# Performance work log

Measured on AMD Instinct MI355X. Metric: run time of the kernel, lower is better.

## Reference

```python
import jax, jax.numpy as jnp
import numpy as np

N_NODES = 50000


def _sage_layer(x, edges, W_neigh, W_self, b):
    """HeteroGraphConv(sum) of per-relation DGL SAGEConv(mean).

    x:        [N, F_in] node features (single node type)
    edges:    [R, 2, E] int (src, dst) per relation
    W_neigh:  [R, F_in, F_out], W_self: [R, F_in, F_out], b: [R, F_out]
    returns:  [N, F_out]
    """
    N = x.shape[0]
    R = edges.shape[0]
    out = jnp.zeros((N, W_neigh.shape[-1]), dtype=x.dtype)
    for r in range(R):  # small fixed number of relation types
        src = edges[r, 0]
        dst = edges[r, 1]
        # mean-aggregate neighbor features onto dst
        s = jax.ops.segment_sum(x[src], dst, num_segments=N)          # [N, F_in]
        deg = jax.ops.segment_sum(jnp.ones_like(dst, dtype=x.dtype), dst,
                                  num_segments=N)                     # [N]
        mean = s / jnp.maximum(deg, 1.0)[:, None]                     # zero-deg -> 0
        # SAGEConv(mean): fc_self(h_dst) + fc_neigh(mean_neigh) + bias
        out = out + x @ W_self[r] + mean @ W_neigh[r] + b[r]
    return out


def setup_inputs() -> dict:
    key = jax.random.key(0)
    ks = jax.random.split(key, 10)
    F_in, H, O, R, E = 128, 128, 64, 2, 800000
    scale_in = 1.0 / np.sqrt(F_in)
    scale_h = 1.0 / np.sqrt(H)
    return {
        "x": jax.random.normal(ks[0], (N_NODES, F_in), dtype=jnp.float32),
        "edges": jax.random.randint(ks[1], (R, 2, E), 0, N_NODES, dtype=jnp.int32),
        "neg_edges": jax.random.randint(ks[2], (2, E), 0, N_NODES, dtype=jnp.int32),
        "W_neigh1": jax.random.normal(ks[3], (R, F_in, H), jnp.float32) * scale_in,
        "W_self1": jax.random.normal(ks[4], (R, F_in, H), jnp.float32) * scale_in,
        "b1": jnp.zeros((R, H), jnp.float32),
        "W_neigh2": jax.random.normal(ks[5], (R, H, O), jnp.float32) * scale_h,
        "W_self2": jax.random.normal(ks[6], (R, H, O), jnp.float32) * scale_h,
        "b2": jnp.zeros((R, O), jnp.float32),
    }


def reference(x, edges, neg_edges, W_neigh1, W_self1, b1, W_neigh2, W_self2, b2):
    h = _sage_layer(x, edges, W_neigh1, W_self1, b1)
    h = jax.nn.relu(h)
    h = _sage_layer(h, edges, W_neigh2, W_self2, b2)          # [N, O]
    # HeteroDotProductPredictor: u_dot_v on edges of the scored etype (rel 0)
    pos_score = jnp.sum(h[edges[0, 0]] * h[edges[0, 1]], axis=-1)      # [E]
    neg_score = jnp.sum(h[neg_edges[0]] * h[neg_edges[1]], axis=-1)    # [E_neg]
    return pos_score, neg_score
```

## Files before the change

### kernel.cpp

```cpp
#include <hip/hip_runtime.h>


#define BW 128
#define NBK_MAX 1024
#define EPB 8192

typedef __attribute__((ext_vector_type(8))) short bf16x8;
typedef __attribute__((ext_vector_type(4))) float floatx4;

__device__ __forceinline__ unsigned short f2bf(float f) {
    unsigned u = __float_as_uint(f);
    unsigned r = u + 0x7FFFu + ((u >> 16) & 1u);
    return (unsigned short)(r >> 16);
}
__device__ __forceinline__ unsigned pack2(float a, float b) {
    return (unsigned)f2bf(a) | ((unsigned)f2bf(b) << 16);
}
__device__ __forceinline__ float bflo(unsigned v) { return __uint_as_float(v << 16); }
__device__ __forceinline__ float bfhi(unsigned v) { return __uint_as_float(v & 0xFFFF0000u); }
#define RFL(x) __builtin_amdgcn_readfirstlane(x)

__global__ __launch_bounds__(256) void
bucket_count_kernel(const int* __restrict__ edges, int* __restrict__ bcnt,
                    int NBK, int E)
{
    __shared__ int cnt[2 * NBK_MAX];
    const int rbT = 2 * NBK;
    const int t = threadIdx.x;
    for (int k = t; k < rbT; k += 256) cnt[k] = 0;
    __syncthreads();
    long long start = (long long)blockIdx.x * EPB;
    long long twoE = 2LL * E;
    for (int u = 0; u < EPB / 256; ++u) {
        long long idx = start + u * 256 + t;
        if (idx < twoE) {
            int r = idx >= E;
            int e = (int)(idx - (long long)r * E);
            int d = edges[(size_t)r * 2 * E + E + e];
            atomicAdd(&cnt[r * NBK + (d >> 7)], 1);
        }
    }
    __syncthreads();
    for (int k = t; k < rbT; k += 256)
        if (cnt[k]) atomicAdd(&bcnt[k], cnt[k]);
}

__global__ __launch_bounds__(1024) void
bucket_scan_kernel(const int* __restrict__ bcnt, int* __restrict__ bko,
                   int rbT, int twoE)
{
    __shared__ int sm[1024];
    int t = threadIdx.x;
    int v = (t < rbT) ? bcnt[t] : 0;
    sm[t] = v;
    __syncthreads();
    for (int s = 1; s < 1024; s <<= 1) {
        int u = (t >= s) ? sm[t - s] : 0;
        __syncthreads();
        sm[t] += u;
        __syncthreads();
    }
    if (t < rbT) bko[t] = sm[t] - v;
    if (t == 0) bko[rbT] = twoE;
}

__global__ __launch_bounds__(256) void
partition_kernel(const int* __restrict__ edges, const int* __restrict__ bko,
                 int* __restrict__ gcur, uint2* __restrict__ staging,
                 int NBK, int E)
{
    __shared__ int cnt[2 * NBK_MAX];
    __shared__ int base[2 * NBK_MAX];
    const int rbT = 2 * NBK;
    const int t = threadIdx.x;
    for (int k = t; k < rbT; k += 256) cnt[k] = 0;
    __syncthreads();
    long long start = (long long)blockIdx.x * EPB;
    long long twoE = 2LL * E;
    for (int u = 0; u < EPB / 256; ++u) {
        long long idx = start + u * 256 + t;
        if (idx < twoE) {
            int r = idx >= E;
            int e = (int)(idx - (long long)r * E);
            int d = edges[(size_t)r * 2 * E + E + e];
            atomicAdd(&cnt[r * NBK + (d >> 7)], 1);
        }
    }
    __syncthreads();
    for (int k = t; k < rbT; k += 256) {
        int c0 = cnt[k];
        if (c0) base[k] = bko[k] + atomicAdd(&gcur[k], c0);
        cnt[k] = 0;
    }
    __syncthreads();
    for (int u = 0; u < EPB / 256; ++u) {
        long long idx = start + u * 256 + t;
        if (idx < twoE) {
            int r = idx >= E;
            int e = (int)(idx - (long long)r * E);
            int s = edges[(size_t)r * 2 * E + e];
            int d = edges[(size_t)r * 2 * E + E + e];
            int rb = r * NBK + (d >> 7);
            int pos = atomicAdd(&cnt[rb], 1);
            staging[(size_t)base[rb] + pos] = make_uint2((unsigned)s, (unsigned)d);
        }
    }
}

__global__ __launch_bounds__(256) void
bucket_csr_kernel(const uint2* __restrict__ staging, const int* __restrict__ bko,
                  int* __restrict__ csr, int* __restrict__ off,
                  int NBK, int N)
{
    __shared__ int hist[BW], excl[BW], cur[BW], sc[BW];
    const int rb = blockIdx.x;
    const int r = rb / NBK;
    const int b = rb % NBK;
    const int node0 = b * BW;
    const int nn = min(BW, N - node0);
    const int cbase = bko[rb];
    const int c = bko[rb + 1] - cbase;
    const int t = threadIdx.x;

    if (t < BW) { hist[t] = 0; cur[t] = 0; }
    __syncthreads();
    for (int k = t; k < c; k += 256)
        atomicAdd(&hist[(int)staging[(size_t)cbase + k].y - node0], 1);
    __syncthreads();
    if (t < BW) sc[t] = hist[t];
    __syncthreads();
    for (int s = 1; s < BW; s <<= 1) {
        int v = (t < BW && t >= s) ? sc[t - s] : 0;
        __syncthreads();
        if (t < BW) sc[t] += v;
        __syncthreads();
    }
    if (t < BW) excl[t] = sc[t] - hist[t];
    if (t < nn) off[(size_t)r * N + node0 + t] = cbase + excl[t];
    __syncthreads();
    for (int k = t; k < c; k += 256) {
        uint2 pr = staging[(size_t)cbase + k];
        int l = (int)pr.y - node0;
        int pos = atomicAdd(&cur[l], 1);
        csr[(size_t)cbase + excl[l] + pos] = (int)pr.x;
    }
}

__global__ void cvt_kernel(const float* __restrict__ in,
                           unsigned short* __restrict__ o, int n4)
{
    int t = blockIdx.x * blockDim.x + threadIdx.x;
    if (t >= n4) return;
    float4 v = ((const float4*)in)[t];
    ushort4 r;
    r.x = f2bf(v.x); r.y = f2bf(v.y); r.z = f2bf(v.z); r.w = f2bf(v.w);
    ((ushort4*)o)[t] = r;
}

__global__ void prep_kernel(const float* __restrict__ Ws1, const float* __restrict__ Wn1,
                            const float* __restrict__ b1,
                            const float* __restrict__ Ws2, const float* __restrict__ Wn2,
                            const float* __restrict__ b2,
                            unsigned short* __restrict__ WT1z, unsigned short* __restrict__ WT1a,
                            unsigned short* __restrict__ WT1b, float* __restrict__ bc1,
                            unsigned short* __restrict__ WT2z, unsigned short* __restrict__ WT2a,
                            unsigned short* __restrict__ WT2b, float* __restrict__ bc2)
{
    int t = blockIdx.x * blockDim.x + threadIdx.x;
    if (t < 16384) {
        int n = t >> 7, k = t & 127;
        int in = k * 128 + n;
        WT1z[t] = f2bf(Ws1[in] + Ws1[16384 + in]);
        WT1a[t] = f2bf(Wn1[in]);
        WT1b[t] = f2bf(Wn1[16384 + in]);
    }
    if (t < 8192) {
        int n = t >> 7, k = t & 127;
        int in = k * 64 + n;
        WT2z[t] = f2bf(Ws2[in] + Ws2[8192 + in]);
        WT2a[t] = f2bf(Wn2[in]);
        WT2b[t] = f2bf(Wn2[8192 + in]);
    }
    if (t < 128) bc1[t] = b1[t] + b1[128 + t];
    if (t < 64)  bc2[t] = b2[t] + b2[64 + t];
}

__global__ __launch_bounds__(256) void
agg1_kernel(const unsigned short* __restrict__ xb,
            const int* __restrict__ csr, const int* __restrict__ off,
            unsigned short* __restrict__ m0, unsigned short* __restrict__ m1,
            int N, int twoE)
{
    int w = blockIdx.x * 4 + (threadIdx.x >> 6);
    int lane = threadIdx.x & 63;
    if (w >= N) return;
    const int col = lane * 2;
    const unsigned short* xc = xb + col;

    float sx0 = 0.f, sy0 = 0.f, sx1 = 0.f, sy1 = 0.f;

    int o0 = RFL(off[w]);
    int o1 = RFL(off[w + 1]);
    int d0 = o1 - o0;
    int j = o0;
    for (; j + 15 < o1; j += 16) {
        int s0 = RFL(csr[j]);      int s1 = RFL(csr[j + 1]);
        int s2 = RFL(csr[j + 2]);  int s3 = RFL(csr[j + 3]);
        int s4 = RFL(csr[j + 4]);  int s5 = RFL(csr[j + 5]);
        int s6 = RFL(csr[j + 6]);  int s7 = RFL(csr[j + 7]);
        int s8 = RFL(csr[j + 8]);  int s9 = RFL(csr[j + 9]);
        int sa = RFL(csr[j + 10]); int sb = RFL(csr[j + 11]);
        int sc = RFL(csr[j + 12]); int sd = RFL(csr[j + 13]);
        int se = RFL(csr[j + 14]); int sf = RFL(csr[j + 15]);
        unsigned a0 = *(const unsigned*)(xc + (size_t)s0 * 128);
        unsigned a1 = *(const unsigned*)(xc + (size_t)s1 * 128);
        unsigned a2 = *(const unsigned*)(xc + (size_t)s2 * 128);
        unsigned a3 = *(const unsigned*)(xc + (size_t)s3 * 128);
        unsigned a4 = *(const unsigned*)(xc + (size_t)s4 * 128);
        unsigned a5 = *(const unsigned*)(xc + (size_t)s5 * 128);
        unsigned a6 = *(const unsigned*)(xc + (size_t)s6 * 128);
        unsigned a7 = *(const unsigned*)(xc + (size_t)s7 * 128);
        unsigned a8 = *(const unsigned*)(xc + (size_t)s8 * 128);
        unsigned a9 = *(const unsigned*)(xc + (size_t)s9 * 128);
        unsigned aa = *(const unsigned*)(xc + (size_t)sa * 128);
        unsigned ab = *(const unsigned*)(xc + (size_t)sb * 128);
        unsigned ac = *(const unsigned*)(xc + (size_t)sc * 128);
        unsigned ad = *(const unsigned*)(xc + (size_t)sd * 128);
        unsigned ae = *(const unsigned*)(xc + (size_t)se * 128);
        unsigned af = *(const unsigned*)(xc + (size_t)sf * 128);
        sx0 += (((bflo(a0) + bflo(a1)) + (bflo(a2) + bflo(a3))) +
                ((bflo(a4) + bflo(a5)) + (bflo(a6) + bflo(a7)))) +
               (((bflo(a8) + bflo(a9)) + (bflo(aa) + bflo(ab))) +
                ((bflo(ac) + bflo(ad)) + (bflo(ae) + bflo(af))));
        sy0 += (((bfhi(a0) + bfhi(a1)) + (bfhi(a2) + bfhi(a3))) +
                ((bfhi(a4) + bfhi(a5)) + (bfhi(a6) + bfhi(a7)))) +
               (((bfhi(a8) + bfhi(a9)) + (bfhi(aa) + bfhi(ab))) +
                ((bfhi(ac) + bfhi(ad)) + (bfhi(ae) + bfhi(af))));
    }
    for (; j + 7 < o1; j += 8) {
        int s0 = RFL(csr[j]);     int s1 = RFL(csr[j + 1]);
        int s2 = RFL(csr[j + 2]); int s3 = RFL(csr[j + 3]);
        int s4 = RFL(csr[j + 4]); int s5 = RFL(csr[j + 5]);
        int s6 = RFL(csr[j + 6]); int s7 = RFL(csr[j + 7]);
        unsigned a0 = *(const unsigned*)(xc + (size_t)s0 * 128);
        unsigned a1 = *(const unsigned*)(xc + (size_t)s1 * 128);
        unsigned a2 = *(const unsigned*)(xc + (size_t)s2 * 128);
        unsigned a3 = *(const unsigned*)(xc + (size_t)s3 * 128);
        unsigned a4 = *(const unsigned*)(xc + (size_t)s4 * 128);
        unsigned a5 = *(const unsigned*)(xc + (size_t)s5 * 128);
        unsigned a6 = *(const unsigned*)(xc + (size_t)s6 * 128);
        unsigned a7 = *(const unsigned*)(xc + (size_t)s7 * 128);
        sx0 += ((bflo(a0) + bflo(a1)) + (bflo(a2) + bflo(a3))) +
               ((bflo(a4) + bflo(a5)) + (bflo(a6) + bflo(a7)));
        sy0 += ((bfhi(a0) + bfhi(a1)) + (bfhi(a2) + bfhi(a3))) +
               ((bfhi(a4) + bfhi(a5)) + (bfhi(a6) + bfhi(a7)));
    }
    for (; j < o1; ++j) {
        int s0 = RFL(csr[j]);
        unsigned a = *(const unsigned*)(xc + (size_t)s0 * 128);
        sx0 += bflo(a); sy0 += bfhi(a);
    }

    int p = N + w;
    o0 = RFL(off[p]);
    o1 = (p + 1 < 2 * N) ? RFL(off[p + 1]) : twoE;
    int d1 = o1 - o0;
    j = o0;
    for (; j + 15 < o1; j += 16) {
        int s0 = RFL(csr[j]);      int s1 = RFL(csr[j + 1]);
        int s2 = RFL(csr[j + 2]);  int s3 = RFL(csr[j + 3]);
        int s4 = RFL(csr[j + 4]);  int s5 = RFL(csr[j + 5]);
        int s6 = RFL(csr[j + 6]);  int s7 = RFL(csr[j + 7]);
        int s8 = RFL(csr[j + 8]);  int s9 = RFL(csr[j + 9]);
        int sa = RFL(csr[j + 10]); int sb = RFL(csr[j + 11]);
        int sc = RFL(csr[j + 12]); int sd = RFL(csr[j + 13]);
        int se = RFL(csr[j + 14]); int sf = RFL(csr[j + 15]);
        unsigned a0 = *(const unsigned*)(xc + (size_t)s0 * 128);
        unsigned a1 = *(const unsigned*)(xc + (size_t)s1 * 128);
        unsigned a2 = *(const unsigned*)(xc + (size_t)s2 * 128);
        unsigned a3 = *(const unsigned*)(xc + (size_t)s3 * 128);
        unsigned a4 = *(const unsigned*)(xc + (size_t)s4 * 128);
        unsigned a5 = *(const unsigned*)(xc + (size_t)s5 * 128);
        unsigned a6 = *(const unsigned*)(xc + (size_t)s6 * 128);
        unsigned a7 = *(const unsigned*)(xc + (size_t)s7 * 128);
        unsigned a8 = *(const unsigned*)(xc + (size_t)s8 * 128);
        unsigned a9 = *(const unsigned*)(xc + (size_t)s9 * 128);
        unsigned aa = *(const unsigned*)(xc + (size_t)sa * 128);
        unsigned ab = *(const unsigned*)(xc + (size_t)sb * 128);
        unsigned ac = *(const unsigned*)(xc + (size_t)sc * 128);
        unsigned ad = *(const unsigned*)(xc + (size_t)sd * 128);
        unsigned ae = *(const unsigned*)(xc + (size_t)se * 128);
        unsigned af = *(const unsigned*)(xc + (size_t)sf * 128);
        sx1 += (((bflo(a0) + bflo(a1)) + (bflo(a2) + bflo(a3))) +
                ((bflo(a4) + bflo(a5)) + (bflo(a6) + bflo(a7)))) +
               (((bflo(a8) + bflo(a9)) + (bflo(aa) + bflo(ab))) +
                ((bflo(ac) + bflo(ad)) + (bflo(ae) + bflo(af))));
        sy1 += (((bfhi(a0) + bfhi(a1)) + (bfhi(a2) + bfhi(a3))) +
                ((bfhi(a4) + bfhi(a5)) + (bfhi(a6) + bfhi(a7)))) +
               (((bfhi(a8) + bfhi(a9)) + (bfhi(aa) + bfhi(ab))) +
                ((bfhi(ac) + bfhi(ad)) + (bfhi(ae) + bfhi(af))));
    }
    for (; j + 7 < o1; j += 8) {
        int s0 = RFL(csr[j]);     int s1 = RFL(csr[j + 1]);
        int s2 = RFL(csr[j + 2]); int s3 = RFL(csr[j + 3]);
        int s4 = RFL(csr[j + 4]); int s5 = RFL(csr[j + 5]);
        int s6 = RFL(csr[j + 6]); int s7 = RFL(csr[j + 7]);
        unsigned a0 = *(const unsigned*)(xc + (size_t)s0 * 128);
        unsigned a1 = *(const unsigned*)(xc + (size_t)s1 * 128);
        unsigned a2 = *(const unsigned*)(xc + (size_t)s2 * 128);
        unsigned a3 = *(const unsigned*)(xc + (size_t)s3 * 128);
        unsigned a4 = *(const unsigned*)(xc + (size_t)s4 * 128);
        unsigned a5 = *(const unsigned*)(xc + (size_t)s5 * 128);
        unsigned a6 = *(const unsigned*)(xc + (size_t)s6 * 128);
        unsigned a7 = *(const unsigned*)(xc + (size_t)s7 * 128);
        sx1 += ((bflo(a0) + bflo(a1)) + (bflo(a2) + bflo(a3))) +
               ((bflo(a4) + bflo(a5)) + (bflo(a6) + bflo(a7)));
        sy1 += ((bfhi(a0) + bfhi(a1)) + (bfhi(a2) + bfhi(a3))) +
               ((bfhi(a4) + bfhi(a5)) + (bfhi(a6) + bfhi(a7)));
    }
    for (; j < o1; ++j) {
        int s0 = RFL(csr[j]);
        unsigned a = *(const unsigned*)(xc + (size_t)s0 * 128);
        sx1 += bflo(a); sy1 += bfhi(a);
    }

    float inv0 = 1.0f / fmaxf((float)d0, 1.0f);
    float inv1 = 1.0f / fmaxf((float)d1, 1.0f);
    *(unsigned*)(m0 + (size_t)w * 128 + col) = pack2(sx0 * inv0, sy0 * inv0);
    *(unsigned*)(m1 + (size_t)w * 128 + col) = pack2(sx1 * inv1, sy1 * inv1);
}

__global__ __launch_bounds__(256) void
gemm1_fused_kernel(const unsigned short* __restrict__ xb,
                   const unsigned short* __restrict__ m0,
                   const unsigned short* __restrict__ m1,
                   const unsigned short* __restrict__ WTz,
                   const unsigned short* __restrict__ WTa,
                   const unsigned short* __restrict__ WTb,
                   const float* __restrict__ bias,
                   unsigned short* __restrict__ h1b, int N)
{
    __shared__ float eb[64][129];

    const int tid = threadIdx.x;
    const int wave = tid >> 6;
    const int lane = tid & 63;
    const int m = lane & 15;
    const int quad = lane >> 4;

    floatx4 acc[8];
    const floatx4 z4 = {0.f, 0.f, 0.f, 0.f};
#pragma unroll
    for (int t = 0; t < 8; ++t) acc[t] = z4;

    int arow = blockIdx.x * 64 + wave * 16 + m;
    if (arow >= N) arow = N - 1;
    const size_t abase = (size_t)arow * 128 + quad * 8;

#pragma unroll
    for (int s = 0; s < 4; ++s) {
        bf16x8 ax = *(const bf16x8*)(xb + abase + s * 32);
        bf16x8 a0 = *(const bf16x8*)(m0 + abase + s * 32);
        bf16x8 a1 = *(const bf16x8*)(m1 + abase + s * 32);
#pragma unroll
        for (int t = 0; t < 8; ++t) {
            const size_t bo = (size_t)(t * 16 + m) * 128 + s * 32 + quad * 8;
            acc[t] = __builtin_amdgcn_mfma_f32_16x16x32_bf16(
                ax, *(const bf16x8*)(WTz + bo), acc[t], 0, 0, 0);
            acc[t] = __builtin_amdgcn_mfma_f32_16x16x32_bf16(
                a0, *(const bf16x8*)(WTa + bo), acc[t], 0, 0, 0);
            acc[t] = __builtin_amdgcn_mfma_f32_16x16x32_bf16(
                a1, *(const bf16x8*)(WTb + bo), acc[t], 0, 0, 0);
        }
    }

#pragma unroll
    for (int t = 0; t < 8; ++t)
#pragma unroll
        for (int i = 0; i < 4; ++i)
            eb[wave * 16 + quad * 4 + i][t * 16 + m] = acc[t][i];
    __syncthreads();

#pragma unroll
    for (int j = 0; j < 4; ++j) {
        int lr = wave * 16 + j * 4 + quad;
        int grow = blockIdx.x * 64 + lr;
        if (grow < N) {
#pragma unroll
            for (int i = 0; i < 2; ++i) {
                int c0 = (i * 16 + m) * 4;
                float v0 = fmaxf(eb[lr][c0 + 0] + bias[c0 + 0], 0.0f);
                float v1 = fmaxf(eb[lr][c0 + 1] + bias[c0 + 1], 0.0f);
                float v2 = fmaxf(eb[lr][c0 + 2] + bias[c0 + 2], 0.0f);
                float v3 = fmaxf(eb[lr][c0 + 3] + bias[c0 + 3], 0.0f);
                ushort4 u;
                u.x = f2bf(v0); u.y = f2bf(v1); u.z = f2bf(v2); u.w = f2bf(v3);
                *(ushort4*)(h1b + (size_t)grow * 128 + c0) = u;
            }
        }
    }
}

__global__ __launch_bounds__(256) void
gemm2_fused_kernel(const unsigned short* __restrict__ Ab,
                   const unsigned short* __restrict__ WTz,
                   const unsigned short* __restrict__ WTa,
                   const unsigned short* __restrict__ WTb,
                   const float* __restrict__ bias,
                   float* __restrict__ zf,
                   unsigned short* __restrict__ ya, unsigned short* __restrict__ yb,
                   int N)
{
    __shared__ float eb[64][65];

    const int tid = threadIdx.x;
    const int wave = tid >> 6;
    const int lane = tid & 63;
    const int m = lane & 15;
    const int quad = lane >> 4;

    floatx4 accz[4], acca[4], accb[4];
    const floatx4 z4 = {0.f, 0.f, 0.f, 0.f};
#pragma unroll
    for (int t = 0; t < 4; ++t) { accz[t] = z4; acca[t] = z4; accb[t] = z4; }

    int arow = blockIdx.x * 64 + wave * 16 + m;
    if (arow >= N) arow = N - 1;
    const unsigned short* aptr = Ab + (size_t)arow * 128 + quad * 8;

#pragma unroll
    for (int s = 0; s < 4; ++s) {
        bf16x8 a = *(const bf16x8*)(aptr + s * 32);
#pragma unroll
        for (int t = 0; t < 4; ++t) {
            const size_t bo = (size_t)(t * 16 + m) * 128 + s * 32 + quad * 8;
            accz[t] = __builtin_amdgcn_mfma_f32_16x16x32_bf16(
                a, *(const bf16x8*)(WTz + bo), accz[t], 0, 0, 0);
            acca[t] = __builtin_amdgcn_mfma_f32_16x16x32_bf16(
                a, *(const bf16x8*)(WTa + bo), acca[t], 0, 0, 0);
            accb[t] = __builtin_amdgcn_mfma_f32_16x16x32_bf16(
                a, *(const bf16x8*)(WTb + bo), accb[t], 0, 0, 0);
        }
    }

#pragma unroll
    for (int t = 0; t < 4; ++t)
#pragma unroll
        for (int i = 0; i < 4; ++i)
            eb[wave * 16 + quad * 4 + i][t * 16 + m] = accz[t][i];
    __syncthreads();
#pragma unroll
    for (int j = 0; j < 4; ++j) {
        int lr = wave * 16 + j * 4 + quad;
        int gr = blockIdx.x * 64 + lr;
        if (gr < N) {
            int c0 = m * 4;
            float4 o;
            o.x = eb[lr][c0 + 0] + bias[c0 + 0];
            o.y = eb[lr][c0 + 1] + bias[c0 + 1];
            o.z = eb[lr][c0 + 2] + bias[c0 + 2];
            o.w = eb[lr][c0 + 3] + bias[c0 + 3];
            *(float4*)(zf + (size_t)gr * 64 + c0) = o;
        }
    }
    __syncthreads();

#pragma unroll
    for (int t = 0; t < 4; ++t)
#pragma unroll
        for (int i = 0; i < 4; ++i)
            eb[wave * 16 + quad * 4 + i][t * 16 + m] = acca[t][i];
    __syncthreads();
#pragma unroll
    for (int j = 0; j < 4; ++j) {
        int lr = wave * 16 + j * 4 + quad;
        int gr = blockIdx.x * 64 + lr;
        if (gr < N) {
            int c0 = m * 4;
            ushort4 u;
            u.x = f2bf(eb[lr][c0 + 0]); u.y = f2bf(eb[lr][c0 + 1]);
            u.z = f2bf(eb[lr][c0 + 2]); u.w = f2bf(eb[lr][c0 + 3]);
            *(ushort4*)(ya + (size_t)gr * 64 + c0) = u;
        }
    }
    __syncthreads();

#pragma unroll
    for (int t = 0; t < 4; ++t)
#pragma unroll
        for (int i = 0; i < 4; ++i)
            eb[wave * 16 + quad * 4 + i][t * 16 + m] = accb[t][i];
    __syncthreads();
#pragma unroll
    for (int j = 0; j < 4; ++j) {
        int lr = wave * 16 + j * 4 + quad;
        int gr = blockIdx.x * 64 + lr;
        if (gr < N) {
            int c0 = m * 4;
            ushort4 u;
            u.x = f2bf(eb[lr][c0 + 0]); u.y = f2bf(eb[lr][c0 + 1]);
            u.z = f2bf(eb[lr][c0 + 2]); u.w = f2bf(eb[lr][c0 + 3]);
            *(ushort4*)(yb + (size_t)gr * 64 + c0) = u;
        }
    }
}

__global__ __launch_bounds__(256) void
agg2_kernel(const unsigned short* __restrict__ t0,
            const unsigned short* __restrict__ t1,
            const float* __restrict__ z2,
            const int* __restrict__ csr, const int* __restrict__ off,
            unsigned short* __restrict__ h2b, int N, int twoE)
{
    int w = blockIdx.x * 4 + (threadIdx.x >> 6);
    int lane = threadIdx.x & 63;
    if (w >= N) return;
    const int half = lane >> 5;
    const int col = (lane & 31) * 2;

    float sx0 = 0.f, sy0 = 0.f, sx1 = 0.f, sy1 = 0.f;
    int o0 = RFL(off[w]);
    int o1 = RFL(off[w + 1]);
    int d0 = o1 - o0;
    int j = o0 + half;
    for (; j + 6 < o1; j += 8) {
        int s0 = csr[j], s1 = csr[j + 2], s2 = csr[j + 4], s3 = csr[j + 6];
        unsigned a0 = *(const unsigned*)(t0 + (size_t)s0 * 64 + col);
        unsigned a1 = *(const unsigned*)(t0 + (size_t)s1 * 64 + col);
        unsigned a2 = *(const unsigned*)(t0 + (size_t)s2 * 64 + col);
        unsigned a3 = *(const unsigned*)(t0 + (size_t)s3 * 64 + col);
        sx0 += (bflo(a0) + bflo(a1)) + (bflo(a2) + bflo(a3));
        sy0 += (bfhi(a0) + bfhi(a1)) + (bfhi(a2) + bfhi(a3));
    }
    for (; j < o1; j += 2) {
        unsigned a = *(const unsigned*)(t0 + (size_t)csr[j] * 64 + col);
        sx0 += bflo(a); sy0 += bfhi(a);
    }
    int p = N + w;
    o0 = RFL(off[p]);
    o1 = (p + 1 < 2 * N) ? RFL(off[p + 1]) : twoE;
    int d1 = o1 - o0;
    j = o0 + half;
    for (; j + 6 < o1; j += 8) {
        int s0 = csr[j], s1 = csr[j + 2], s2 = csr[j + 4], s3 = csr[j + 6];
        unsigned a0 = *(const unsigned*)(t1 + (size_t)s0 * 64 + col);
        unsigned a1 = *(const unsigned*)(t1 + (size_t)s1 * 64 + col);
        unsigned a2 = *(const unsigned*)(t1 + (size_t)s2 * 64 + col);
        unsigned a3 = *(const unsigned*)(t1 + (size_t)s3 * 64 + col);
        sx1 += (bflo(a0) + bflo(a1)) + (bflo(a2) + bflo(a3));
        sy1 += (bfhi(a0) + bfhi(a1)) + (bfhi(a2) + bfhi(a3));
    }
    for (; j < o1; j += 2) {
        unsigned a = *(const unsigned*)(t1 + (size_t)csr[j] * 64 + col);
        sx1 += bflo(a); sy1 += bfhi(a);
    }
    sx0 += __shfl_xor(sx0, 32);
    sy0 += __shfl_xor(sy0, 32);
    sx1 += __shfl_xor(sx1, 32);
    sy1 += __shfl_xor(sy1, 32);
    if (half == 0) {
        float inv0 = 1.0f / fmaxf((float)d0, 1.0f);
        float inv1 = 1.0f / fmaxf((float)d1, 1.0f);
        float2 z = *(const float2*)(z2 + (size_t)w * 64 + col);
        float hx = z.x + sx0 * inv0 + sx1 * inv1;
        float hy = z.y + sy0 * inv0 + sy1 * inv1;
        *(unsigned*)(h2b + (size_t)w * 64 + col) = pack2(hx, hy);
    }
}

__global__ __launch_bounds__(256) void
score_kernel(const unsigned short* __restrict__ h,
             const int* __restrict__ edges, const int* __restrict__ neg,
             float* __restrict__ out, int E, int En)
{
    int t = blockIdx.x * blockDim.x + threadIdx.x;
    int e = t >> 3;
    int c = t & 7;
    if (e >= E + En) return;
    int sI, dI, oI;
    if (e < E) { sI = edges[e]; dI = edges[E + e]; oI = e; }
    else { int en = e - E; sI = neg[en]; dI = neg[En + en]; oI = E + en; }
    uint4 va = *(const uint4*)(h + (size_t)sI * 64 + c * 8);
    uint4 vb = *(const uint4*)(h + (size_t)dI * 64 + c * 8);
    float s = 0.0f;
    s = fmaf(bflo(va.x), bflo(vb.x), s);
    s = fmaf(bfhi(va.x), bfhi(vb.x), s);
    s = fmaf(bflo(va.y), bflo(vb.y), s);
    s = fmaf(bfhi(va.y), bfhi(vb.y), s);
    s = fmaf(bflo(va.z), bflo(vb.z), s);
    s = fmaf(bfhi(va.z), bfhi(vb.z), s);
    s = fmaf(bflo(va.w), bflo(vb.w), s);
    s = fmaf(bfhi(va.w), bfhi(vb.w), s);
    s += __shfl_xor(s, 1);
    s += __shfl_xor(s, 2);
    s += __shfl_xor(s, 4);
    if (c == 0) out[oI] = s;
}

extern "C" void kernel_launch(void* const* d_in, const int* in_sizes, int n_in,
                              void* d_out, int out_size, void* d_ws, size_t ws_size,
                              hipStream_t stream)
{
    const float* x     = (const float*)d_in[0];
    const int*   edges = (const int*)d_in[1];
    const int*   neg   = (const int*)d_in[2];
    const float* Wn1   = (const float*)d_in[3];
    const float* Ws1   = (const float*)d_in[4];
    const float* b1    = (const float*)d_in[5];
    const float* Wn2   = (const float*)d_in[6];
    const float* Ws2   = (const float*)d_in[7];
    const float* b2    = (const float*)d_in[8];
    float* out = (float*)d_out;

    const int Fin = 128, R = 2;
    const int N  = in_sizes[0] / Fin;
    const int E  = in_sizes[1] / (R * 2);
    const int En = in_sizes[2] / 2;
    const int twoE = 2 * E;
    const int NBK = (N + BW - 1) / BW;
    const int rbT = 2 * NBK;

    const size_t nb128 = (size_t)N * 128 * sizeof(unsigned short);
    char* p = (char*)d_ws;

    uint2* staging = (uint2*)p;
    float* z2      = (float*)p;
    {
        size_t r0 = (size_t)twoE * sizeof(uint2);
        size_t r1 = (size_t)N * 64 * sizeof(float);
        p += (r0 > r1 ? r0 : r1);
    }
    unsigned short* m0  = (unsigned short*)p; p += nb128;
    unsigned short* m1  = (unsigned short*)p; p += nb128;
    unsigned short* xb  = (unsigned short*)p; p += nb128;
    unsigned short* h1b = (unsigned short*)p; p += nb128;
    unsigned short* WT1z = (unsigned short*)p; p += 16384 * 2;
    unsigned short* WT1a = (unsigned short*)p; p += 16384 * 2;
    unsigned short* WT1b = (unsigned short*)p; p += 16384 * 2;
    unsigned short* WT2z = (unsigned short*)p; p += 8192 * 2;
    unsigned short* WT2a = (unsigned short*)p; p += 8192 * 2;
    unsigned short* WT2b = (unsigned short*)p; p += 8192 * 2;
    float* bc1 = (float*)p; p += 128 * sizeof(float);
    float* bc2 = (float*)p; p += 64 * sizeof(float);
    int* bcnt = (int*)p; p += (size_t)2 * NBK_MAX * sizeof(int);
    int* gcur = (int*)p; p += (size_t)2 * NBK_MAX * sizeof(int);
    int* bko  = (int*)p; p += ((size_t)2 * NBK_MAX + 1) * sizeof(int);
    int* off  = (int*)p; p += (size_t)2 * N * sizeof(int);
    int* csr  = (int*)p;

    unsigned short* t0  = m0;
    unsigned short* t1  = m0 + (size_t)N * 64;
    unsigned short* h2b = m1;

    const int BS = 256;
    const int edge_blocks = (twoE + EPB - 1) / EPB;
    const int gx = (N + 63) / 64;

    hipMemsetAsync(bcnt, 0, (size_t)4 * NBK_MAX * sizeof(int), stream);
    bucket_count_kernel<<<edge_blocks, BS, 0, stream>>>(edges, bcnt, NBK, E);
    bucket_scan_kernel<<<1, 1024, 0, stream>>>(bcnt, bko, rbT, twoE);
    partition_kernel<<<edge_blocks, BS, 0, stream>>>(edges, bko, gcur, staging, NBK, E);
    bucket_csr_kernel<<<rbT, BS, 0, stream>>>(staging, bko, csr, off, NBK, N);

    cvt_kernel<<<(N * 32 + BS - 1) / BS, BS, 0, stream>>>(x, xb, N * 32);
    prep_kernel<<<(16384 + BS - 1) / BS, BS, 0, stream>>>(
        Ws1, Wn1, b1, Ws2, Wn2, b2,
        WT1z, WT1a, WT1b, bc1, WT2z, WT2a, WT2b, bc2);

    agg1_kernel<<<(N + 3) / 4, BS, 0, stream>>>(xb, csr, off, m0, m1, N, twoE);
    gemm1_fused_kernel<<<gx, BS, 0, stream>>>(xb, m0, m1, WT1z, WT1a, WT1b,
                                              bc1, h1b, N);

    gemm2_fused_kernel<<<gx, BS, 0, stream>>>(h1b, WT2z, WT2a, WT2b, bc2,
                                              z2, t0, t1, N);
    agg2_kernel<<<(N + 3) / 4, BS, 0, stream>>>(t0, t1, z2, csr, off, h2b, N, twoE);

    score_kernel<<<((E + En) * 8 + BS - 1) / BS, BS, 0, stream>>>(
        h2b, edges, neg, out, E, En);
}
```

Measured before the change: 382.8 us.

## Tile node features into 32-column slabs for cache-local gathers in aggregation and scoring

Node features, neighbor means and final embeddings are stored column-tiled, as 32-column slabs of N rows, instead of row-major. The aggregation and scoring kernels gain a grid dimension over slabs, so each pass gathers from a smaller working set that fits better in cache. Within agg1, each wavefront now handles four edges at a time across lane quarters and combines them with shuffles. Scoring splits each dot product across two slabs and accumulates with float atomics into a zeroed output, which adds a memset, atomics and redundant index loads.

```diff
diff --git a/kernel.cpp b/kernel.cpp
--- a/kernel.cpp
+++ b/kernel.cpp
@@ -147,14 +147,18 @@
 }
 
 __global__ void cvt_kernel(const float* __restrict__ in,
-                           unsigned short* __restrict__ o, int n4)
+                           unsigned short* __restrict__ xbt, int N)
 {
     int t = blockIdx.x * blockDim.x + threadIdx.x;
-    if (t >= n4) return;
+    if (t >= N * 32) return;
+    int row = t >> 5;
+    int c4 = (t & 31) * 4;
     float4 v = ((const float4*)in)[t];
     ushort4 r;
     r.x = f2bf(v.x); r.y = f2bf(v.y); r.z = f2bf(v.z); r.w = f2bf(v.w);
-    ((ushort4*)o)[t] = r;
+    int tile = c4 >> 5;
+    int tcol = c4 & 31;
+    *(ushort4*)(xbt + ((size_t)tile * N + row) * 32 + tcol) = r;
 }
 
 __global__ void prep_kernel(const float* __restrict__ Ws1, const float* __restrict__ Wn1,
@@ -186,16 +190,17 @@
 }
 
 __global__ __launch_bounds__(256) void
-agg1_kernel(const unsigned short* __restrict__ xb,
+agg1_kernel(const unsigned short* __restrict__ xbt,
             const int* __restrict__ csr, const int* __restrict__ off,
-            unsigned short* __restrict__ m0, unsigned short* __restrict__ m1,
+            unsigned short* __restrict__ m0t, unsigned short* __restrict__ m1t,
             int N, int twoE)
 {
     int w = blockIdx.x * 4 + (threadIdx.x >> 6);
     int lane = threadIdx.x & 63;
     if (w >= N) return;
-    const int col = lane * 2;
-    const unsigned short* xc = xb + col;
+    const int q = lane >> 4;
+    const int col = (lane & 15) * 2;
+    const unsigned short* xc = xbt + (size_t)blockIdx.y * N * 32 + col;
 
     float sx0 = 0.f, sy0 = 0.f, sx1 = 0.f, sy1 = 0.f;
 
@@ -204,60 +209,25 @@
     int d0 = o1 - o0;
     int j = o0;
     for (; j + 15 < o1; j += 16) {
-        int s0 = RFL(csr[j]);      int s1 = RFL(csr[j + 1]);
-        int s2 = RFL(csr[j + 2]);  int s3 = RFL(csr[j + 3]);
-        int s4 = RFL(csr[j + 4]);  int s5 = RFL(csr[j + 5]);
-        int s6 = RFL(csr[j + 6]);  int s7 = RFL(csr[j + 7]);
-        int s8 = RFL(csr[j + 8]);  int s9 = RFL(csr[j + 9]);
-        int sa = RFL(csr[j + 10]); int sb = RFL(csr[j + 11]);
-        int sc = RFL(csr[j + 12]); int sd = RFL(csr[j + 13]);
-        int se = RFL(csr[j + 14]); int sf = RFL(csr[j + 15]);
-        unsigned a0 = *(const unsigned*)(xc + (size_t)s0 * 128);
-        unsigned a1 = *(const unsigned*)(xc + (size_t)s1 * 128);
-        unsigned a2 = *(const unsigned*)(xc + (size_t)s2 * 128);
-        unsigned a3 = *(const unsigned*)(xc + (size_t)s3 * 128);
-        unsigned a4 = *(const unsigned*)(xc + (size_t)s4 * 128);
-        unsigned a5 = *(const unsigned*)(xc + (size_t)s5 * 128);
-        unsigned a6 = *(const unsigned*)(xc + (size_t)s6 * 128);
-        unsigned a7 = *(const unsigned*)(xc + (size_t)s7 * 128);
-        unsigned a8 = *(const unsigned*)(xc + (size_t)s8 * 128);
-        unsigned a9 = *(const unsigned*)(xc + (size_t)s9 * 128);
-        unsigned aa = *(const unsigned*)(xc + (size_t)sa * 128);
-        unsigned ab = *(const unsigned*)(xc + (size_t)sb * 128);
-        unsigned ac = *(const unsigned*)(xc + (size_t)sc * 128);
-        unsigned ad = *(const unsigned*)(xc + (size_t)sd * 128);
-        unsigned ae = *(const unsigned*)(xc + (size_t)se * 128);
-        unsigned af = *(const unsigned*)(xc + (size_t)sf * 128);
-        sx0 += (((bflo(a0) + bflo(a1)) + (bflo(a2) + bflo(a3))) +
-                ((bflo(a4) + bflo(a5)) + (bflo(a6) + bflo(a7)))) +
-               (((bflo(a8) + bflo(a9)) + (bflo(aa) + bflo(ab))) +
-                ((bflo(ac) + bflo(ad)) + (bflo(ae) + bflo(af))));
-        sy0 += (((bfhi(a0) + bfhi(a1)) + (bfhi(a2) + bfhi(a3))) +
-                ((bfhi(a4) + bfhi(a5)) + (bfhi(a6) + bfhi(a7)))) +
-               (((bfhi(a8) + bfhi(a9)) + (bfhi(aa) + bfhi(ab))) +
-                ((bfhi(ac) + bfhi(ad)) + (bfhi(ae) + bfhi(af))));
-    }
-    for (; j + 7 < o1; j += 8) {
-        int s0 = RFL(csr[j]);     int s1 = RFL(csr[j + 1]);
-        int s2 = RFL(csr[j + 2]); int s3 = RFL(csr[j + 3]);
-        int s4 = RFL(csr[j + 4]); int s5 = RFL(csr[j + 5]);
-        int s6 = RFL(csr[j + 6]); int s7 = RFL(csr[j + 7]);
-        unsigned a0 = *(const unsigned*)(xc + (size_t)s0 * 128);
-        unsigned a1 = *(const unsigned*)(xc + (size_t)s1 * 128);
-        unsigned a2 = *(const unsigned*)(xc + (size_t)s2 * 128);
-        unsigned a3 = *(const unsigned*)(xc + (size_t)s3 * 128);
-        unsigned a4 = *(const unsigned*)(xc + (size_t)s4 * 128);
-        unsigned a5 = *(const unsigned*)(xc + (size_t)s5 * 128);
-        unsigned a6 = *(const unsigned*)(xc + (size_t)s6 * 128);
-        unsigned a7 = *(const unsigned*)(xc + (size_t)s7 * 128);
-        sx0 += ((bflo(a0) + bflo(a1)) + (bflo(a2) + bflo(a3))) +
-               ((bflo(a4) + bflo(a5)) + (bflo(a6) + bflo(a7)));
-        sy0 += ((bfhi(a0) + bfhi(a1)) + (bfhi(a2) + bfhi(a3))) +
-               ((bfhi(a4) + bfhi(a5)) + (bfhi(a6) + bfhi(a7)));
-    }
-    for (; j < o1; ++j) {
-        int s0 = RFL(csr[j]);
-        unsigned a = *(const unsigned*)(xc + (size_t)s0 * 128);
+        int r0 = csr[j + q];
+        int r1 = csr[j + 4 + q];
+        int r2 = csr[j + 8 + q];
+        int r3 = csr[j + 12 + q];
+        unsigned a0 = *(const unsigned*)(xc + (size_t)r0 * 32);
+        unsigned a1 = *(const unsigned*)(xc + (size_t)r1 * 32);
+        unsigned a2 = *(const unsigned*)(xc + (size_t)r2 * 32);
+        unsigned a3 = *(const unsigned*)(xc + (size_t)r3 * 32);
+        sx0 += (bflo(a0) + bflo(a1)) + (bflo(a2) + bflo(a3));
+        sy0 += (bfhi(a0) + bfhi(a1)) + (bfhi(a2) + bfhi(a3));
+    }
+    for (; j + 3 < o1; j += 4) {
+        int r = csr[j + q];
+        unsigned a = *(const unsigned*)(xc + (size_t)r * 32);
+        sx0 += bflo(a); sy0 += bfhi(a);
+    }
+    if (j < o1 && q < o1 - j) {
+        int r = csr[j + q];
+        unsigned a = *(const unsigned*)(xc + (size_t)r * 32);
         sx0 += bflo(a); sy0 += bfhi(a);
     }
 
@@ -267,73 +237,45 @@
     int d1 = o1 - o0;
     j = o0;
     for (; j + 15 < o1; j += 16) {
-        int s0 = RFL(csr[j]);      int s1 = RFL(csr[j + 1]);
-        int s2 = RFL(csr[j + 2]);  int s3 = RFL(csr[j + 3]);
-        int s4 = RFL(csr[j + 4]);  int s5 = RFL(csr[j + 5]);
-        int s6 = RFL(csr[j + 6]);  int s7 = RFL(csr[j + 7]);
-        int s8 = RFL(csr[j + 8]);  int s9 = RFL(csr[j + 9]);
-        int sa = RFL(csr[j + 10]); int sb = RFL(csr[j + 11]);
-        int sc = RFL(csr[j + 12]); int sd = RFL(csr[j + 13]);
-        int se = RFL(csr[j + 14]); int sf = RFL(csr[j + 15]);
-        unsigned a0 = *(const unsigned*)(xc + (size_t)s0 * 128);
-        unsigned a1 = *(const unsigned*)(xc + (size_t)s1 * 128);
-        unsigned a2 = *(const unsigned*)(xc + (size_t)s2 * 128);
-        unsigned a3 = *(const unsigned*)(xc + (size_t)s3 * 128);
-        unsigned a4 = *(const unsigned*)(xc + (size_t)s4 * 128);
-        unsigned a5 = *(const unsigned*)(xc + (size_t)s5 * 128);
-        unsigned a6 = *(const unsigned*)(xc + (size_t)s6 * 128);
-        unsigned a7 = *(const unsigned*)(xc + (size_t)s7 * 128);
-        unsigned a8 = *(const unsigned*)(xc + (size_t)s8 * 128);
-        unsigned a9 = *(const unsigned*)(xc + (size_t)s9 * 128);
-        unsigned aa = *(const unsigned*)(xc + (size_t)sa * 128);
-        unsigned ab = *(const unsigned*)(xc + (size_t)sb * 128);
-        unsigned ac = *(const unsigned*)(xc + (size_t)sc * 128);
-        unsigned ad = *(const unsigned*)(xc + (size_t)sd * 128);
-        unsigned ae = *(const unsigned*)(xc + (size_t)se * 128);
-        unsigned af = *(const unsigned*)(xc + (size_t)sf * 128);
-        sx1 += (((bflo(a0) + bflo(a1)) + (bflo(a2) + bflo(a3))) +
-                ((bflo(a4) + bflo(a5)) + (bflo(a6) + bflo(a7)))) +
-               (((bflo(a8) + bflo(a9)) + (bflo(aa) + bflo(ab))) +
-                ((bflo(ac) + bflo(ad)) + (bflo(ae) + bflo(af))));
-        sy1 += (((bfhi(a0) + bfhi(a1)) + (bfhi(a2) + bfhi(a3))) +
-                ((bfhi(a4) + bfhi(a5)) + (bfhi(a6) + bfhi(a7)))) +
-               (((bfhi(a8) + bfhi(a9)) + (bfhi(aa) + bfhi(ab))) +
-                ((bfhi(ac) + bfhi(ad)) + (bfhi(ae) + bfhi(af))));
-    }
-    for (; j + 7 < o1; j += 8) {
-        int s0 = RFL(csr[j]);     int s1 = RFL(csr[j + 1]);
-        int s2 = RFL(csr[j + 2]); int s3 = RFL(csr[j + 3]);
-        int s4 = RFL(csr[j + 4]); int s5 = RFL(csr[j + 5]);
-        int s6 = RFL(csr[j + 6]); int s7 = RFL(csr[j + 7]);
-        unsigned a0 = *(const unsigned*)(xc + (size_t)s0 * 128);
-        unsigned a1 = *(const unsigned*)(xc + (size_t)s1 * 128);
-        unsigned a2 = *(const unsigned*)(xc + (size_t)s2 * 128);
-        unsigned a3 = *(const unsigned*)(xc + (size_t)s3 * 128);
-        unsigned a4 = *(const unsigned*)(xc + (size_t)s4 * 128);
-        unsigned a5 = *(const unsigned*)(xc + (size_t)s5 * 128);
-        unsigned a6 = *(const unsigned*)(xc + (size_t)s6 * 128);
-        unsigned a7 = *(const unsigned*)(xc + (size_t)s7 * 128);
-        sx1 += ((bflo(a0) + bflo(a1)) + (bflo(a2) + bflo(a3))) +
-               ((bflo(a4) + bflo(a5)) + (bflo(a6) + bflo(a7)));
-        sy1 += ((bfhi(a0) + bfhi(a1)) + (bfhi(a2) + bfhi(a3))) +
-               ((bfhi(a4) + bfhi(a5)) + (bfhi(a6) + bfhi(a7)));
-    }
-    for (; j < o1; ++j) {
-        int s0 = RFL(csr[j]);
-        unsigned a = *(const unsigned*)(xc + (size_t)s0 * 128);
+        int r0 = csr[j + q];
+        int r1 = csr[j + 4 + q];
+        int r2 = csr[j + 8 + q];
+        int r3 = csr[j + 12 + q];
+        unsigned a0 = *(const unsigned*)(xc + (size_t)r0 * 32);
+        unsigned a1 = *(const unsigned*)(xc + (size_t)r1 * 32);
+        unsigned a2 = *(const unsigned*)(xc + (size_t)r2 * 32);
+        unsigned a3 = *(const unsigned*)(xc + (size_t)r3 * 32);
+        sx1 += (bflo(a0) + bflo(a1)) + (bflo(a2) + bflo(a3));
+        sy1 += (bfhi(a0) + bfhi(a1)) + (bfhi(a2) + bfhi(a3));
+    }
+    for (; j + 3 < o1; j += 4) {
+        int r = csr[j + q];
+        unsigned a = *(const unsigned*)(xc + (size_t)r * 32);
         sx1 += bflo(a); sy1 += bfhi(a);
     }
-
-    float inv0 = 1.0f / fmaxf((float)d0, 1.0f);
-    float inv1 = 1.0f / fmaxf((float)d1, 1.0f);
-    *(unsigned*)(m0 + (size_t)w * 128 + col) = pack2(sx0 * inv0, sy0 * inv0);
-    *(unsigned*)(m1 + (size_t)w * 128 + col) = pack2(sx1 * inv1, sy1 * inv1);
-}
-
-__global__ __launch_bounds__(256) void
-gemm1_fused_kernel(const unsigned short* __restrict__ xb,
-                   const unsigned short* __restrict__ m0,
-                   const unsigned short* __restrict__ m1,
+    if (j < o1 && q < o1 - j) {
+        int r = csr[j + q];
+        unsigned a = *(const unsigned*)(xc + (size_t)r * 32);
+        sx1 += bflo(a); sy1 += bfhi(a);
+    }
+
+    sx0 += __shfl_xor(sx0, 16); sy0 += __shfl_xor(sy0, 16);
+    sx0 += __shfl_xor(sx0, 32); sy0 += __shfl_xor(sy0, 32);
+    sx1 += __shfl_xor(sx1, 16); sy1 += __shfl_xor(sy1, 16);
+    sx1 += __shfl_xor(sx1, 32); sy1 += __shfl_xor(sy1, 32);
+    if (q == 0) {
+        float inv0 = 1.0f / fmaxf((float)d0, 1.0f);
+        float inv1 = 1.0f / fmaxf((float)d1, 1.0f);
+        size_t o = ((size_t)blockIdx.y * N + w) * 32 + col;
+        *(unsigned*)(m0t + o) = pack2(sx0 * inv0, sy0 * inv0);
+        *(unsigned*)(m1t + o) = pack2(sx1 * inv1, sy1 * inv1);
+    }
+}
+
+__global__ __launch_bounds__(256) void
+gemm1_fused_kernel(const unsigned short* __restrict__ xbt,
+                   const unsigned short* __restrict__ m0t,
+                   const unsigned short* __restrict__ m1t,
                    const unsigned short* __restrict__ WTz,
                    const unsigned short* __restrict__ WTa,
                    const unsigned short* __restrict__ WTb,
@@ -355,13 +297,13 @@
 
     int arow = blockIdx.x * 64 + wave * 16 + m;
     if (arow >= N) arow = N - 1;
-    const size_t abase = (size_t)arow * 128 + quad * 8;
 
 #pragma unroll
     for (int s = 0; s < 4; ++s) {
-        bf16x8 ax = *(const bf16x8*)(xb + abase + s * 32);
-        bf16x8 a0 = *(const bf16x8*)(m0 + abase + s * 32);
-        bf16x8 a1 = *(const bf16x8*)(m1 + abase + s * 32);
+        const size_t tb = ((size_t)s * N + arow) * 32 + quad * 8;
+        bf16x8 ax = *(const bf16x8*)(xbt + tb);
+        bf16x8 a0 = *(const bf16x8*)(m0t + tb);
+        bf16x8 a1 = *(const bf16x8*)(m1t + tb);
 #pragma unroll
         for (int t = 0; t < 8; ++t) {
             const size_t bo = (size_t)(t * 16 + m) * 128 + s * 32 + quad * 8;
@@ -510,7 +452,8 @@
             const unsigned short* __restrict__ t1,
             const float* __restrict__ z2,
             const int* __restrict__ csr, const int* __restrict__ off,
-            unsigned short* __restrict__ h2b, int N, int twoE)
+            unsigned short* __restrict__ h2bt,
+            int N, int twoE)
 {
     int w = blockIdx.x * 4 + (threadIdx.x >> 6);
     int lane = threadIdx.x & 63;
@@ -564,14 +507,16 @@
         float2 z = *(const float2*)(z2 + (size_t)w * 64 + col);
         float hx = z.x + sx0 * inv0 + sx1 * inv1;
         float hy = z.y + sy0 * inv0 + sy1 * inv1;
-        *(unsigned*)(h2b + (size_t)w * 64 + col) = pack2(hx, hy);
-    }
-}
-
-__global__ __launch_bounds__(256) void
-score_kernel(const unsigned short* __restrict__ h,
+        int tile = col >> 5;
+        *(unsigned*)(h2bt + ((size_t)tile * N + w) * 32 + (col & 31)) =
+            pack2(hx, hy);
+    }
+}
+
+__global__ __launch_bounds__(256) void
+score_kernel(const unsigned short* __restrict__ h2bt,
              const int* __restrict__ edges, const int* __restrict__ neg,
-             float* __restrict__ out, int E, int En)
+             float* __restrict__ out, int E, int En, int N)
 {
     int t = blockIdx.x * blockDim.x + threadIdx.x;
     int e = t >> 3;
@@ -580,21 +525,18 @@
     int sI, dI, oI;
     if (e < E) { sI = edges[e]; dI = edges[E + e]; oI = e; }
     else { int en = e - E; sI = neg[en]; dI = neg[En + en]; oI = E + en; }
-    uint4 va = *(const uint4*)(h + (size_t)sI * 64 + c * 8);
-    uint4 vb = *(const uint4*)(h + (size_t)dI * 64 + c * 8);
+    const unsigned short* hb = h2bt + (size_t)blockIdx.y * N * 32;
+    uint2 va = *(const uint2*)(hb + (size_t)sI * 32 + c * 4);
+    uint2 vb = *(const uint2*)(hb + (size_t)dI * 32 + c * 4);
     float s = 0.0f;
     s = fmaf(bflo(va.x), bflo(vb.x), s);
     s = fmaf(bfhi(va.x), bfhi(vb.x), s);
     s = fmaf(bflo(va.y), bflo(vb.y), s);
     s = fmaf(bfhi(va.y), bfhi(vb.y), s);
-    s = fmaf(bflo(va.z), bflo(vb.z), s);
-    s = fmaf(bfhi(va.z), bfhi(vb.z), s);
-    s = fmaf(bflo(va.w), bflo(vb.w), s);
-    s = fmaf(bfhi(va.w), bfhi(vb.w), s);
     s += __shfl_xor(s, 1);
     s += __shfl_xor(s, 2);
     s += __shfl_xor(s, 4);
-    if (c == 0) out[oI] = s;
+    if (c == 0) atomicAdd(&out[oI], s);
 }
 
 extern "C" void kernel_launch(void* const* d_in, const int* in_sizes, int n_in,
@@ -630,9 +572,9 @@
         size_t r1 = (size_t)N * 64 * sizeof(float);
         p += (r0 > r1 ? r0 : r1);
     }
-    unsigned short* m0  = (unsigned short*)p; p += nb128;
-    unsigned short* m1  = (unsigned short*)p; p += nb128;
-    unsigned short* xb  = (unsigned short*)p; p += nb128;
+    unsigned short* m0t = (unsigned short*)p; p += nb128;
+    unsigned short* m1t = (unsigned short*)p; p += nb128;
+    unsigned short* xbt = (unsigned short*)p; p += nb128;
     unsigned short* h1b = (unsigned short*)p; p += nb128;
     unsigned short* WT1z = (unsigned short*)p; p += 16384 * 2;
     unsigned short* WT1a = (unsigned short*)p; p += 16384 * 2;
@@ -648,9 +590,9 @@
     int* off  = (int*)p; p += (size_t)2 * N * sizeof(int);
     int* csr  = (int*)p;
 
-    unsigned short* t0  = m0;
-    unsigned short* t1  = m0 + (size_t)N * 64;
-    unsigned short* h2b = m1;
+    unsigned short* t0   = m0t;
+    unsigned short* t1   = m0t + (size_t)N * 64;
+    unsigned short* h2bt = m1t;
 
     const int BS = 256;
     const int edge_blocks = (twoE + EPB - 1) / EPB;
@@ -662,19 +604,25 @@
     partition_kernel<<<edge_blocks, BS, 0, stream>>>(edges, bko, gcur, staging, NBK, E);
     bucket_csr_kernel<<<rbT, BS, 0, stream>>>(staging, bko, csr, off, NBK, N);
 
-    cvt_kernel<<<(N * 32 + BS - 1) / BS, BS, 0, stream>>>(x, xb, N * 32);
+    cvt_kernel<<<(N * 32 + BS - 1) / BS, BS, 0, stream>>>(x, xbt, N);
     prep_kernel<<<(16384 + BS - 1) / BS, BS, 0, stream>>>(
         Ws1, Wn1, b1, Ws2, Wn2, b2,
         WT1z, WT1a, WT1b, bc1, WT2z, WT2a, WT2b, bc2);
 
-    agg1_kernel<<<(N + 3) / 4, BS, 0, stream>>>(xb, csr, off, m0, m1, N, twoE);
-    gemm1_fused_kernel<<<gx, BS, 0, stream>>>(xb, m0, m1, WT1z, WT1a, WT1b,
+    {
+        dim3 g((N + 3) / 4, 4);
+        agg1_kernel<<<g, BS, 0, stream>>>(xbt, csr, off, m0t, m1t, N, twoE);
+    }
+    gemm1_fused_kernel<<<gx, BS, 0, stream>>>(xbt, m0t, m1t, WT1z, WT1a, WT1b,
                                               bc1, h1b, N);
 
     gemm2_fused_kernel<<<gx, BS, 0, stream>>>(h1b, WT2z, WT2a, WT2b, bc2,
                                               z2, t0, t1, N);
-    agg2_kernel<<<(N + 3) / 4, BS, 0, stream>>>(t0, t1, z2, csr, off, h2b, N, twoE);
-
-    score_kernel<<<((E + En) * 8 + BS - 1) / BS, BS, 0, stream>>>(
-        h2b, edges, neg, out, E, En);
-}
+    agg2_kernel<<<(N + 3) / 4, BS, 0, stream>>>(t0, t1, z2, csr, off, h2bt, N, twoE);
+
+    hipMemsetAsync(out, 0, (size_t)(E + En) * sizeof(float), stream);
+    {
+        dim3 g(((E + En) * 8 + BS - 1) / BS, 2);
+        score_kernel<<<g, BS, 0, stream>>>(h2bt, edges, neg, out, E, En, N);
+    }
+}
```

Measured after the change: 478.9 us. +25.1%, slower.
